# Optimization experiments

Hardware: AMD Instinct MI355X
Metric: run time of the kernel (lower is better)

## Reference

```python
import jax, jax.numpy as jnp
import numpy as np

OBS, ACT, H, B = 128, 32, 64, 32768
TMAX = 8  # max variable-length GRU steps: (15-1)//2+1 == 15//2+1 == 8
CENTER = 7


def gru_last(x_seq, valid, Wih, Whh, bih, bhh):
    """torch nn.GRU cell, masked scan; returns final hidden at each true length.
    x_seq: (B, TMAX, D), valid: (B, TMAX) bool. Gate order r, z, n."""
    Bn = x_seq.shape[0]
    h0 = jnp.zeros((Bn, Whh.shape[1]), x_seq.dtype)

    def step(h, inp):
        xt, vt = inp  # (B, D), (B,)
        gi = xt @ Wih.T + bih
        gh = h @ Whh.T + bhh
        ir, iz, inn = jnp.split(gi, 3, axis=-1)
        hr, hz, hn = jnp.split(gh, 3, axis=-1)
        r = jax.nn.sigmoid(ir + hr)
        zg = jax.nn.sigmoid(iz + hz)
        n = jnp.tanh(inn + r * hn)
        hnew = (1.0 - zg) * n + zg * h
        h = jnp.where(vt[:, None], hnew, h)
        return h, None

    h, _ = jax.lax.scan(step, h0, (jnp.swapaxes(x_seq, 0, 1), valid.T))
    return h


def setup_inputs() -> dict:
    key = jax.random.key(0)
    ks = jax.random.split(key, 20)
    def p(k, shape, s=0.05):
        return jax.random.normal(k, shape, jnp.float32) * s
    D = OBS + ACT
    return dict(
        obs_chunk=jax.random.normal(ks[0], (B, 15, OBS), jnp.float32),
        act_chunk=jax.random.normal(ks[1], (B, 15, ACT), jnp.float32),
        ln_g=jnp.ones((3,), jnp.float32), ln_b=jnp.zeros((3,), jnp.float32),
        dw1=p(ks[2], (16, 3)), db1=jnp.zeros((16,), jnp.float32),
        dw2=p(ks[3], (8, 16)), db2=jnp.zeros((8,), jnp.float32),
        dw3=p(ks[4], (14, 8)), db3=jnp.zeros((14,), jnp.float32),
        Wih_f=p(ks[5], (3 * H, D)), Whh_f=p(ks[6], (3 * H, H)),
        bih_f=jnp.zeros((3 * H,), jnp.float32), bhh_f=jnp.zeros((3 * H,), jnp.float32),
        Wih_b=p(ks[7], (3 * H, D)), Whh_b=p(ks[8], (3 * H, H)),
        bih_b=jnp.zeros((3 * H,), jnp.float32), bhh_b=jnp.zeros((3 * H,), jnp.float32),
        mw1=p(ks[9], (H, 2 * H)), mb1=jnp.zeros((H,), jnp.float32),
        mw2=p(ks[10], (H, H)), mb2=jnp.zeros((H,), jnp.float32),
        mu_w=p(ks[11], (H, H)), mu_b=jnp.zeros((H,), jnp.float32),
        lv_w=p(ks[12], (H, H)), lv_b=jnp.zeros((H,), jnp.float32),
    )


def reference(obs_chunk, act_chunk, ln_g, ln_b, dw1, db1, dw2, db2, dw3, db3,
              Wih_f, Whh_f, bih_f, bhh_f, Wih_b, Whh_b, bih_b, bhh_b,
              mw1, mb1, mw2, mb2, mu_w, mu_b, lv_w, lv_b):
    C = CENTER
    # --- DynamicTimeWindow features ---
    obs_t = obs_chunk[:, C]  # (B, OBS)
    pr = jax.nn.softmax(obs_t, axis=-1)
    entropy = -jnp.sum(pr * jnp.log(pr + 1e-8), axis=-1, keepdims=True)
    diffs = jnp.stack([jnp.linalg.norm(obs_chunk[:, C - k] - obs_chunk[:, C - k - 1], axis=-1)
                       for k in range(3)], axis=1)
    roc = diffs.mean(axis=1, keepdims=True)
    act_prev = act_chunk[:, C - 1]
    md = max(obs_t.shape[-1], act_prev.shape[-1])
    op = jnp.pad(obs_t, ((0, 0), (0, md - obs_t.shape[-1])))
    ap = jnp.pad(act_prev, ((0, 0), (0, md - act_prev.shape[-1])))
    oc = op - op.mean(axis=1, keepdims=True)
    ac = ap - ap.mean(axis=1, keepdims=True)
    denom = (jnp.linalg.norm(oc, axis=1, keepdims=True)
             * jnp.linalg.norm(ac, axis=1, keepdims=True) + 1e-8)
    corr = jnp.sum(oc * ac, axis=1, keepdims=True) / denom
    f = jnp.concatenate([entropy, roc, corr], axis=1)  # (B, 3)
    mean = f.mean(axis=-1, keepdims=True)
    var = f.var(axis=-1, keepdims=True)  # biased, matches torch LayerNorm
    fn = (f - mean) / jnp.sqrt(var + 1e-5) * ln_g + ln_b
    h1 = jax.nn.relu(fn @ dw1.T + db1)
    h2 = jax.nn.relu(h1 @ dw2.T + db2)
    logits = h2 @ dw3.T + db3  # (B, 14)
    widx = jnp.argmax(logits, axis=1)  # test_mode: argmax of softmax == argmax of logits
    wl = widx + 2  # window_len in [2, 15]
    idxs = jnp.arange(15)[None, :]
    start = (C - (wl - 1) // 2)[:, None]
    end = (C + wl // 2 + 1)[:, None]
    mask = ((idxs >= start) & (idxs < end)).astype(obs_chunk.dtype)  # (B, 15)
    x = jnp.concatenate([obs_chunk, act_chunk], axis=-1) * mask[..., None]  # (B, 15, D)
    # --- BiGRU over variable-length windows ---
    len_f = (wl - 1) // 2 + 1  # (B,)
    len_b = wl // 2 + 1
    t = jnp.arange(TMAX)
    idx_f = C - len_f[:, None] + 1 + t[None, :]  # left-aligned forward window
    idx_b = C + len_b[:, None] - 1 - t[None, :]  # reversed backward window
    seq_f = jnp.take_along_axis(x, idx_f[..., None], axis=1)  # (B, 8, D)
    seq_b = jnp.take_along_axis(x, idx_b[..., None], axis=1)
    vf = t[None, :] < len_f[:, None]
    vb = t[None, :] < len_b[:, None]
    h_f = gru_last(seq_f, vf, Wih_f, Whh_f, bih_f, bhh_f)  # (B, H)
    h_b = gru_last(seq_b, vb, Wih_b, Whh_b, bih_b, bhh_b)
    comb = jnp.concatenate([h_f, h_b], axis=1)  # (B, 2H)
    zenc = jax.nn.relu(comb @ mw1.T + mb1) @ mw2.T + mb2
    mu = zenc @ mu_w.T + mu_b
    sigma = jnp.exp(0.5 * (zenc @ lv_w.T + lv_b))
    z = mu  # test_mode=True
    return (z, mu, sigma)
```

## Files before the change

kernel.cpp:

```cpp
#include <hip/hip_runtime.h>

#define OBS 128
#define ACTD 32
#define DIMX 160
#define HID 64
#define NBATCH 32768
#define TMAXX 8
#define CTR 7
#define NPOS 15

typedef short bf16x8 __attribute__((ext_vector_type(8)));
typedef float f32x4 __attribute__((ext_vector_type(4)));

#define MFMA(a,b,c) __builtin_amdgcn_mfma_f32_16x16x32_bf16((a),(b),(c),0,0,0)

#define CTRL_BYTE 262144
#define SIDX_BYTE 278528
#define SIDX_CAP  66048
#define WB_BYTE   542720
#define COMB_BYTE 755712
#define NCB 64
#define EPB 512
#define HEAD_W_OFF 10752
#define TOTAL_SLOTS 13312

__device__ __forceinline__ unsigned short f2bf(float f) {
  unsigned u = __float_as_uint(f);
  return (unsigned short)((u + 0x7FFFu + ((u >> 16) & 1u)) >> 16);
}
__device__ __forceinline__ unsigned cvtpk(float a, float b) {
  unsigned r;
  asm("v_cvt_pk_bf16_f32 %0, %1, %2" : "=v"(r) : "v"(a), "v"(b));
  return r;
}

__device__ __forceinline__ float wsum(float v) {
#pragma unroll
  for (int s = 1; s < 64; s <<= 1) v += __shfl_xor(v, s);
  return v;
}
__device__ __forceinline__ float wmax(float v) {
#pragma unroll
  for (int s = 1; s < 64; s <<= 1) v = fmaxf(v, __shfl_xor(v, s));
  return v;
}

__global__ __launch_bounds__(256) void k_prep(
    const float* __restrict__ Wih_f, const float* __restrict__ Whh_f,
    const float* __restrict__ Wih_b, const float* __restrict__ Whh_b,
    const float* __restrict__ mw1, const float* __restrict__ mw2,
    const float* __restrict__ mu_w, const float* __restrict__ lv_w,
    unsigned short* __restrict__ dst) {
  int slot = blockIdx.x * 256 + threadIdx.x;
  if (slot >= TOTAL_SLOTS) return;
  const float* src;
  if (slot < HEAD_W_OFF) {
    int d = slot / 5376, r = slot % 5376;
    int f = r >> 8, rw = r & 255;
    int w = rw >> 6, lane = rw & 63;
    int col = lane & 15, kgrp = lane >> 4;
    int row = 16 * w + col;
    if (f < 15) {
      int g = f / 5, kf = f % 5;
      const float* W = d ? Wih_b : Wih_f;
      src = W + (size_t)(g * 64 + row) * 160 + kf * 32 + kgrp * 8;
    } else {
      int f2 = f - 15, g = f2 >> 1, kh = f2 & 1;
      const float* W = d ? Whh_b : Whh_f;
      src = W + (size_t)(g * 64 + row) * 64 + kh * 32 + kgrp * 8;
    }
  } else {
    int s2 = slot - HEAD_W_OFF;
    int f = s2 >> 8, rw = s2 & 255;
    int w = rw >> 6, lane = rw & 63;
    int col = lane & 15, kgrp = lane >> 4;
    int gr = 16 * w + col;
    if (f < 4)      src = mw1 + (size_t)gr * 128 + f * 32 + kgrp * 8;
    else if (f < 6) src = mw2 + (size_t)gr * 64 + (f - 4) * 32 + kgrp * 8;
    else if (f < 8) src = mu_w + (size_t)gr * 64 + (f - 6) * 32 + kgrp * 8;
    else            src = lv_w + (size_t)gr * 64 + (f - 8) * 32 + kgrp * 8;
  }
  unsigned short* o = dst + (size_t)slot * 8;
#pragma unroll
  for (int i = 0; i < 8; i++) o[i] = f2bf(src[i]);
}

__global__ __launch_bounds__(256) void k_decide(
    const float* __restrict__ obs, const float* __restrict__ act,
    const float* __restrict__ ln_g, const float* __restrict__ ln_b,
    const float* __restrict__ dw1, const float* __restrict__ db1,
    const float* __restrict__ dw2, const float* __restrict__ db2,
    const float* __restrict__ dw3, const float* __restrict__ db3,
    int* __restrict__ lens) {
  int b = blockIdx.x * 4 + (threadIdx.x >> 6);
  int l = threadIdx.x & 63;
  const float* o7 = obs + ((size_t)b * NPOS + CTR) * OBS;
  const float* o6 = o7 - OBS;
  const float* o5 = o7 - 2 * OBS;
  const float* o4 = o7 - 3 * OBS;
  float x0 = o7[l], x1 = o7[l + 64];
  float y60 = o6[l], y61 = o6[l + 64];
  float y50 = o5[l], y51 = o5[l + 64];
  float y40 = o4[l], y41 = o4[l + 64];
  float ap = (l < 32) ? act[((size_t)b * NPOS + 6) * ACTD + l] : 0.0f;

  float m = wmax(fmaxf(x0, x1));
  float e0 = expf(x0 - m), e1 = expf(x1 - m);
  float s = wsum(e0 + e1);
  float inv = 1.0f / s;
  float p0 = e0 * inv, p1 = e1 * inv;
  float ent = -wsum(p0 * logf(p0 + 1e-8f) + p1 * logf(p1 + 1e-8f));

  float d0 = wsum((x0 - y60) * (x0 - y60) + (x1 - y61) * (x1 - y61));
  float d1 = wsum((y60 - y50) * (y60 - y50) + (y61 - y51) * (y61 - y51));
  float d2 = wsum((y50 - y40) * (y50 - y40) + (y51 - y41) * (y51 - y41));
  float roc = (sqrtf(d0) + sqrtf(d1) + sqrtf(d2)) / 3.0f;

  float sop = wsum(x0 + x1);
  float sop2 = wsum(x0 * x0 + x1 * x1);
  float sap = wsum(ap);
  float sap2 = wsum(ap * ap);
  float dotoa = wsum(ap * x0);
  float mo = sop / 128.0f, ma = sap / 128.0f;
  float num = dotoa - 128.0f * mo * ma;
  float oc2 = fmaxf(sop2 - 128.0f * mo * mo, 0.0f);
  float ac2 = fmaxf(sap2 - 128.0f * ma * ma, 0.0f);
  float corr = num / (sqrtf(oc2) * sqrtf(ac2) + 1e-8f);

  float f0 = ent, f1 = roc, f2 = corr;
  float mean = (f0 + f1 + f2) / 3.0f;
  float v0 = f0 - mean, v1 = f1 - mean, v2 = f2 - mean;
  float var = (v0 * v0 + v1 * v1 + v2 * v2) / 3.0f;
  float sd = sqrtf(var + 1e-5f);
  float fn0 = v0 / sd * ln_g[0] + ln_b[0];
  float fn1 = v1 / sd * ln_g[1] + ln_b[1];
  float fn2 = v2 / sd * ln_g[2] + ln_b[2];

  float h1[16];
#pragma unroll
  for (int i = 0; i < 16; i++) {
    float a = db1[i] + fn0 * dw1[i * 3] + fn1 * dw1[i * 3 + 1] + fn2 * dw1[i * 3 + 2];
    h1[i] = fmaxf(a, 0.0f);
  }
  float h2[8];
#pragma unroll
  for (int i = 0; i < 8; i++) {
    float a = db2[i];
#pragma unroll
    for (int j = 0; j < 16; j++) a += h1[j] * dw2[i * 16 + j];
    h2[i] = fmaxf(a, 0.0f);
  }
  float best = -3.0e38f;
  int bi = 0;
#pragma unroll
  for (int i = 0; i < 14; i++) {
    float a = db3[i];
#pragma unroll
    for (int j = 0; j < 8; j++) a += h2[j] * dw3[i * 8 + j];
    if (a > best) { best = a; bi = i; }
  }
  int wl = bi + 2;
  if (l == 0) {
    lens[b] = (wl - 1) / 2 + 1;
    lens[NBATCH + b] = wl / 2 + 1;
  }
}

__global__ __launch_bounds__(256) void k_count(
    const int* __restrict__ lens, int* __restrict__ ctrl) {
  __shared__ int hist[16];
  const int tid = threadIdx.x, blk = blockIdx.x;
  if (tid < 16) hist[tid] = 0;
  __syncthreads();
#pragma unroll
  for (int j = 0; j < 2; j++) {
    int e = blk * EPB + j * 256 + tid;
    atomicAdd(&hist[lens[e] - 1], 1);
    atomicAdd(&hist[8 + lens[NBATCH + e] - 1], 1);
  }
  __syncthreads();
  if (tid < 16) ctrl[32 + 1024 + blk * 16 + tid] = hist[tid];
}

__global__ void k_scan(int* __restrict__ ctrl) {
  __shared__ int tot[16];
  __shared__ int pss[17];
  const int tid = threadIdx.x;
  const int* bh = ctrl + 32 + 1024;
  int* bb = ctrl + 32;
  if (tid < 16) {
    int s = 0;
    for (int blk = 0; blk < NCB; blk++) {
      bb[blk * 16 + tid] = s;
      s += bh[blk * 16 + tid];
    }
    tot[tid] = s;
  }
  __syncthreads();
  if (tid == 0) {
    int acc = 0;
    for (int k = 0; k < 16; k++) {
      pss[k] = acc;
      acc += (tot[k] + 31) & ~31;
    }
    pss[16] = acc;
    for (int k = 0; k < 17; k++) ctrl[k] = pss[k];
  }
  __syncthreads();
  if (tid < 16) {
    for (int blk = 0; blk < NCB; blk++) bb[blk * 16 + tid] += pss[tid];
  }
}

__global__ __launch_bounds__(256) void k_place(
    const int* __restrict__ lens, const int* __restrict__ ctrl,
    int* __restrict__ sidx) {
  __shared__ int hist[16];
  __shared__ int base[16];
  const int tid = threadIdx.x, blk = blockIdx.x;
  if (tid < 16) {
    hist[tid] = 0;
    base[tid] = ctrl[32 + blk * 16 + tid];
  }
  __syncthreads();
#pragma unroll
  for (int j = 0; j < 2; j++) {
    int e = blk * EPB + j * 256 + tid;
    int binf = lens[e] - 1;
    sidx[base[binf] + atomicAdd(&hist[binf], 1)] = e;
    int binb = 8 + lens[NBATCH + e] - 1;
    sidx[base[binb] + atomicAdd(&hist[binb], 1)] = e;
  }
}

__global__ __launch_bounds__(256, 2) void k_gru(
    const float* __restrict__ obs, const float* __restrict__ act,
    const int* __restrict__ ctrl, const int* __restrict__ sidx,
    const unsigned short* __restrict__ wbf,
    const float* __restrict__ bih_f, const float* __restrict__ bhh_f,
    const float* __restrict__ bih_b, const float* __restrict__ bhh_b,
    unsigned short* __restrict__ comb) {
  __shared__ unsigned short Xl[2][32 * 168];
  __shared__ unsigned short Hl[2][32 * 72];
  __shared__ int ei[32];

  const int tid = threadIdx.x;
  const int p = blockIdx.x * 32;
  const int* ps = ctrl;
  if (p >= ps[16]) return;
  int bin = 0;
#pragma unroll
  for (int k = 1; k < 16; k++) bin += (p >= ps[k]) ? 1 : 0;
  const int d = bin >> 3;
  const int len = (bin & 7) + 1;

  if (tid < 32) ei[tid] = sidx[p + tid];
  __syncthreads();

  const int w = tid >> 6, l = tid & 63;
  const int col = l & 15, kgrp = l >> 4;
  const int gr = 16 * w + col;

  const float* bih = d ? bih_b : bih_f;
  const float* bhh = d ? bhh_b : bhh_f;
  const float bias_r = bih[gr] + bhh[gr];
  const float bias_z = bih[64 + gr] + bhh[64 + gr];
  const float bias_in = bih[128 + gr];
  const float bias_hn = bhh[128 + gr];

  const unsigned short* fb = wbf + ((size_t)d * 5376 + tid) * 8;
  bf16x8 wr[5], wz[5], wn[5];
#pragma unroll
  for (int kf = 0; kf < 5; kf++) {
    wr[kf] = *(const bf16x8*)(fb + (size_t)kf * 2048);
    wz[kf] = *(const bf16x8*)(fb + (size_t)(5 + kf) * 2048);
    wn[kf] = *(const bf16x8*)(fb + (size_t)(10 + kf) * 2048);
  }
  bf16x8 vr[2], vz[2], vn[2];
#pragma unroll
  for (int kh = 0; kh < 2; kh++) {
    vr[kh] = *(const bf16x8*)(fb + (size_t)(15 + kh) * 2048);
    vz[kh] = *(const bf16x8*)(fb + (size_t)(17 + kh) * 2048);
    vn[kh] = *(const bf16x8*)(fb + (size_t)(19 + kh) * 2048);
  }

  const int p0 = d ? (CTR + len - 1) : (CTR - len + 1);
  const float* pst[5];
  int sstr[5], sdo[5];
#pragma unroll
  for (int it = 0; it < 5; it++) {
    int i = tid + it * 256;
    int eloc = i / 40;
    int q = i - eloc * 40;
    int eg = ei[eloc];
    if (eg < 0) eg = ei[0];
    if (q < 32) {
      pst[it] = obs + ((size_t)eg * NPOS + p0) * OBS + q * 4;
      sstr[it] = d ? -OBS : OBS;
    } else {
      pst[it] = act + ((size_t)eg * NPOS + p0) * ACTD + (q - 32) * 4;
      sstr[it] = d ? -ACTD : ACTD;
    }
    sdo[it] = eloc * 168 + ((q < 32) ? q * 4 : 128 + (q - 32) * 4);
  }
  float4 sv[5];

  auto stage_issue = [&](int t1) {
#pragma unroll
    for (int it = 0; it < 5; it++)
      sv[it] = *(const float4*)(pst[it] + (ptrdiff_t)t1 * sstr[it]);
  };
  auto stage_commit = [&](int buf) {
#pragma unroll
    for (int it = 0; it < 5; it++) {
      uint2 pk;
      pk.x = cvtpk(sv[it].x, sv[it].y);
      pk.y = cvtpk(sv[it].z, sv[it].w);
      *(uint2*)(&Xl[buf][sdo[it]]) = pk;
    }
  };

  stage_issue(0);
  stage_commit(0);
  __syncthreads();

  f32x4 hreg[2];
#pragma unroll
  for (int m = 0; m < 2; m++) hreg[m] = (f32x4){0.f, 0.f, 0.f, 0.f};

  for (int t = 0; t < len; t++) {
    const int cur = t & 1, nxt = cur ^ 1;
    const bool more = (t + 1 < len);
    if (more) stage_issue(t + 1);

    f32x4 ar[2], az[2], ain[2], ahn[2];
#pragma unroll
    for (int m = 0; m < 2; m++) {
      ar[m] = (f32x4){0.f, 0.f, 0.f, 0.f};
      az[m] = (f32x4){0.f, 0.f, 0.f, 0.f};
      ain[m] = (f32x4){0.f, 0.f, 0.f, 0.f};
      ahn[m] = (f32x4){0.f, 0.f, 0.f, 0.f};
    }
#pragma unroll
    for (int kf = 0; kf < 5; kf++) {
#pragma unroll
      for (int m = 0; m < 2; m++) {
        bf16x8 xa = *(const bf16x8*)(&Xl[cur][(col + 16 * m) * 168 + kf * 32 + kgrp * 8]);
        ar[m] = MFMA(xa, wr[kf], ar[m]);
        az[m] = MFMA(xa, wz[kf], az[m]);
        ain[m] = MFMA(xa, wn[kf], ain[m]);
      }
    }
    if (t > 0) {
#pragma unroll
      for (int kh = 0; kh < 2; kh++) {
#pragma unroll
        for (int m = 0; m < 2; m++) {
          bf16x8 ha = *(const bf16x8*)(&Hl[cur][(col + 16 * m) * 72 + kh * 32 + kgrp * 8]);
          ar[m] = MFMA(ha, vr[kh], ar[m]);
          az[m] = MFMA(ha, vz[kh], az[m]);
          ahn[m] = MFMA(ha, vn[kh], ahn[m]);
        }
      }
    }

#pragma unroll
    for (int m = 0; m < 2; m++) {
      float hvv[4];
#pragma unroll
      for (int r = 0; r < 4; r++) {
        float air = ar[m][r] + bias_r;
        float aiz = az[m][r] + bias_z;
        float rg = __builtin_amdgcn_rcpf(1.0f + __expf(-air));
        float zg = __builtin_amdgcn_rcpf(1.0f + __expf(-aiz));
        float nn = fmaf(rg, ahn[m][r] + bias_hn, ain[m][r] + bias_in);
        float th = fmaf(-2.0f, __builtin_amdgcn_rcpf(__expf(2.0f * nn) + 1.0f), 1.0f);
        float hp = hreg[m][r];
        float hv = fmaf(zg, hp - th, th);
        hreg[m][r] = hv;
        hvv[r] = hv;
      }
      if (more) {
        unsigned ua = cvtpk(hvv[0], hvv[1]);
        unsigned ub = cvtpk(hvv[2], hvv[3]);
        int row0 = (16 * m + kgrp * 4) * 72 + gr;
        Hl[nxt][row0] = (unsigned short)ua;
        Hl[nxt][row0 + 72] = (unsigned short)(ua >> 16);
        Hl[nxt][row0 + 144] = (unsigned short)ub;
        Hl[nxt][row0 + 216] = (unsigned short)(ub >> 16);
      }
    }

    if (more) {
      stage_commit(nxt);
      __syncthreads();
    }
  }

#pragma unroll
  for (int m = 0; m < 2; m++) {
#pragma unroll
    for (int r = 0; r < 4; r++) {
      int eg = ei[16 * m + kgrp * 4 + r];
      if (eg >= 0)
        comb[(size_t)eg * 128 + 64 * d + gr] = f2bf(hreg[m][r]);
    }
  }
}

__global__ __launch_bounds__(256) void k_head(
    const unsigned short* __restrict__ comb, const unsigned short* __restrict__ wbf,
    const float* __restrict__ mb1, const float* __restrict__ mb2,
    const float* __restrict__ mu_b, const float* __restrict__ lv_b,
    float* __restrict__ out) {
  __shared__ unsigned short Cl[64 * 136];
  __shared__ unsigned short Hl[64 * 72];
  __shared__ unsigned short Zl[64 * 72];

  const int tid = threadIdx.x;
  const int w = tid >> 6, l = tid & 63;
  const int col = l & 15, kgrp = l >> 4;
  const int gr = 16 * w + col;
  const int base = blockIdx.x * 64;

  {
    int row = tid >> 2, sq = tid & 3;
    const uint4* src = (const uint4*)(comb + (size_t)(base + row) * 128 + sq * 32);
    uint4* dst = (uint4*)(&Cl[row * 136 + sq * 32]);
#pragma unroll
    for (int j = 0; j < 4; j++) dst[j] = src[j];
  }
  __syncthreads();

  const unsigned short* hfb = wbf + ((size_t)HEAD_W_OFF + tid) * 8;
  const float b1 = mb1[gr], b2v = mb2[gr], bmu = mu_b[gr], blv = lv_b[gr];

  f32x4 t1[4];
#pragma unroll
  for (int m = 0; m < 4; m++) t1[m] = (f32x4){0.f, 0.f, 0.f, 0.f};
#pragma unroll
  for (int kf = 0; kf < 4; kf++) {
    bf16x8 bw = *(const bf16x8*)(hfb + (size_t)kf * 2048);
#pragma unroll
    for (int m = 0; m < 4; m++) {
      bf16x8 ca = *(const bf16x8*)(&Cl[(col + 16 * m) * 136 + kf * 32 + kgrp * 8]);
      t1[m] = MFMA(ca, bw, t1[m]);
    }
  }
#pragma unroll
  for (int m = 0; m < 4; m++) {
#pragma unroll
    for (int r = 0; r < 4; r++) {
      float v = fmaxf(t1[m][r] + b1, 0.0f);
      Hl[(16 * m + kgrp * 4 + r) * 72 + gr] = f2bf(v);
    }
  }
  __syncthreads();

  f32x4 ze[4];
#pragma unroll
  for (int m = 0; m < 4; m++) ze[m] = (f32x4){0.f, 0.f, 0.f, 0.f};
#pragma unroll
  for (int kh = 0; kh < 2; kh++) {
    bf16x8 bw = *(const bf16x8*)(hfb + (size_t)(4 + kh) * 2048);
#pragma unroll
    for (int m = 0; m < 4; m++) {
      bf16x8 ha = *(const bf16x8*)(&Hl[(col + 16 * m) * 72 + kh * 32 + kgrp * 8]);
      ze[m] = MFMA(ha, bw, ze[m]);
    }
  }
#pragma unroll
  for (int m = 0; m < 4; m++) {
#pragma unroll
    for (int r = 0; r < 4; r++) {
      Zl[(16 * m + kgrp * 4 + r) * 72 + gr] = f2bf(ze[m][r] + b2v);
    }
  }
  __syncthreads();

  f32x4 amu[4], alv[4];
#pragma unroll
  for (int m = 0; m < 4; m++) {
    amu[m] = (f32x4){0.f, 0.f, 0.f, 0.f};
    alv[m] = (f32x4){0.f, 0.f, 0.f, 0.f};
  }
#pragma unroll
  for (int kh = 0; kh < 2; kh++) {
    bf16x8 bwm = *(const bf16x8*)(hfb + (size_t)(6 + kh) * 2048);
    bf16x8 bwl = *(const bf16x8*)(hfb + (size_t)(8 + kh) * 2048);
#pragma unroll
    for (int m = 0; m < 4; m++) {
      bf16x8 za = *(const bf16x8*)(&Zl[(col + 16 * m) * 72 + kh * 32 + kgrp * 8]);
      amu[m] = MFMA(za, bwm, amu[m]);
      alv[m] = MFMA(za, bwl, alv[m]);
    }
  }
#pragma unroll
  for (int m = 0; m < 4; m++) {
#pragma unroll
    for (int r = 0; r < 4; r++) {
      int e = 16 * m + kgrp * 4 + r;
      float mu = amu[m][r] + bmu;
      float sg = expf(0.5f * (alv[m][r] + blv));
      size_t o = (size_t)(base + e) * HID + gr;
      out[o] = mu;
      out[(size_t)NBATCH * HID + o] = mu;
      out[2 * (size_t)NBATCH * HID + o] = sg;
    }
  }
}

extern "C" void kernel_launch(void* const* d_in, const int* in_sizes, int n_in,
                              void* d_out, int out_size, void* d_ws, size_t ws_size,
                              hipStream_t stream) {
  const float* obs = (const float*)d_in[0];
  const float* act = (const float*)d_in[1];
  const float* ln_g = (const float*)d_in[2];
  const float* ln_b = (const float*)d_in[3];
  const float* dw1 = (const float*)d_in[4];
  const float* db1 = (const float*)d_in[5];
  const float* dw2 = (const float*)d_in[6];
  const float* db2 = (const float*)d_in[7];
  const float* dw3 = (const float*)d_in[8];
  const float* db3 = (const float*)d_in[9];
  const float* Wih_f = (const float*)d_in[10];
  const float* Whh_f = (const float*)d_in[11];
  const float* bih_f = (const float*)d_in[12];
  const float* bhh_f = (const float*)d_in[13];
  const float* Wih_b = (const float*)d_in[14];
  const float* Whh_b = (const float*)d_in[15];
  const float* bih_b = (const float*)d_in[16];
  const float* bhh_b = (const float*)d_in[17];
  const float* mw1 = (const float*)d_in[18];
  const float* mb1 = (const float*)d_in[19];
  const float* mw2 = (const float*)d_in[20];
  const float* mb2 = (const float*)d_in[21];
  const float* mu_w = (const float*)d_in[22];
  const float* mu_b = (const float*)d_in[23];
  const float* lv_w = (const float*)d_in[24];
  const float* lv_b = (const float*)d_in[25];

  int* lens = (int*)d_ws;
  int* ctrl = (int*)((char*)d_ws + CTRL_BYTE);
  int* sidx = (int*)((char*)d_ws + SIDX_BYTE);
  unsigned short* wbf = (unsigned short*)((char*)d_ws + WB_BYTE);
  unsigned short* comb = (unsigned short*)((char*)d_ws + COMB_BYTE);

  hipMemsetAsync(sidx, 0xFF, SIDX_CAP * sizeof(int), stream);

  k_prep<<<(TOTAL_SLOTS + 255) / 256, 256, 0, stream>>>(
      Wih_f, Whh_f, Wih_b, Whh_b, mw1, mw2, mu_w, lv_w, wbf);
  k_decide<<<NBATCH / 4, 256, 0, stream>>>(obs, act, ln_g, ln_b, dw1, db1, dw2,
                                           db2, dw3, db3, lens);
  k_count<<<NCB, 256, 0, stream>>>(lens, ctrl);
  k_scan<<<1, 64, 0, stream>>>(ctrl);
  k_place<<<NCB, 256, 0, stream>>>(lens, ctrl, sidx);
  k_gru<<<SIDX_CAP / 32, 256, 0, stream>>>(obs, act, ctrl, sidx, wbf, bih_f,
                                           bhh_f, bih_b, bhh_b, comb);
  k_head<<<NBATCH / 64, 256, 0, stream>>>(comb, wbf, mb1, mb2, mu_b, lv_b,
                                          (float*)d_out);
}
```

Measured before the change: 127.0 us.

## Widen GRU tiles to 64 sequences, fill padding in scan, simplify entropy

The GRU kernel now handles 64 sequences per block instead of 32, so each wave runs four MFMA row tiles per preloaded weight fragment. Bins are padded to multiples of 64 to match, and the sidx padding slots are filled with -1 inside k_scan, which replaces the full-buffer memset. The entropy in k_decide is rewritten as log(s) - sum(e*(x-m))/s using fast intrinsics, removing per-element logs. The tradeoffs are doubled LDS and staging registers, which can lower occupancy, more wasted padding rows, and fewer blocks in flight.

```diff
diff --git a/kernel.cpp b/kernel.cpp
--- a/kernel.cpp
+++ b/kernel.cpp
@@ -16,9 +16,9 @@
 
 #define CTRL_BYTE 262144
 #define SIDX_BYTE 278528
-#define SIDX_CAP  66048
-#define WB_BYTE   542720
-#define COMB_BYTE 755712
+#define SIDX_CAP  66560
+#define WB_BYTE   544768
+#define COMB_BYTE 757760
 #define NCB 64
 #define EPB 512
 #define HEAD_W_OFF 10752
@@ -105,11 +105,10 @@
   float ap = (l < 32) ? act[((size_t)b * NPOS + 6) * ACTD + l] : 0.0f;
 
   float m = wmax(fmaxf(x0, x1));
-  float e0 = expf(x0 - m), e1 = expf(x1 - m);
+  float e0 = __expf(x0 - m), e1 = __expf(x1 - m);
   float s = wsum(e0 + e1);
-  float inv = 1.0f / s;
-  float p0 = e0 * inv, p1 = e1 * inv;
-  float ent = -wsum(p0 * logf(p0 + 1e-8f) + p1 * logf(p1 + 1e-8f));
+  float dot = wsum(e0 * (x0 - m) + e1 * (x1 - m));
+  float ent = __logf(s) - dot / s;
 
   float d0 = wsum((x0 - y60) * (x0 - y60) + (x1 - y61) * (x1 - y61));
   float d1 = wsum((y60 - y50) * (y60 - y50) + (y61 - y51) * (y61 - y51));
@@ -182,7 +181,7 @@
   if (tid < 16) ctrl[32 + 1024 + blk * 16 + tid] = hist[tid];
 }
 
-__global__ void k_scan(int* __restrict__ ctrl) {
+__global__ void k_scan(int* __restrict__ ctrl, int* __restrict__ sidx) {
   __shared__ int tot[16];
   __shared__ int pss[17];
   const int tid = threadIdx.x;
@@ -201,7 +200,7 @@
     int acc = 0;
     for (int k = 0; k < 16; k++) {
       pss[k] = acc;
-      acc += (tot[k] + 31) & ~31;
+      acc += (tot[k] + 63) & ~63;
     }
     pss[16] = acc;
     for (int k = 0; k < 17; k++) ctrl[k] = pss[k];
@@ -209,6 +208,11 @@
   __syncthreads();
   if (tid < 16) {
     for (int blk = 0; blk < NCB; blk++) bb[blk * 16 + tid] += pss[tid];
+  }
+  __syncthreads();
+  for (int k = 0; k < 16; k++) {
+    int s = pss[k] + tot[k], e2 = pss[k + 1];
+    for (int i = s + tid; i < e2; i += 64) sidx[i] = -1;
   }
 }
 
@@ -240,12 +244,12 @@
     const float* __restrict__ bih_f, const float* __restrict__ bhh_f,
     const float* __restrict__ bih_b, const float* __restrict__ bhh_b,
     unsigned short* __restrict__ comb) {
-  __shared__ unsigned short Xl[2][32 * 168];
-  __shared__ unsigned short Hl[2][32 * 72];
-  __shared__ int ei[32];
+  __shared__ unsigned short Xl[2][64 * 168];
+  __shared__ unsigned short Hl[2][64 * 72];
+  __shared__ int ei[64];
 
   const int tid = threadIdx.x;
-  const int p = blockIdx.x * 32;
+  const int p = blockIdx.x * 64;
   const int* ps = ctrl;
   if (p >= ps[16]) return;
   int bin = 0;
@@ -254,7 +258,7 @@
   const int d = bin >> 3;
   const int len = (bin & 7) + 1;
 
-  if (tid < 32) ei[tid] = sidx[p + tid];
+  if (tid < 64) ei[tid] = sidx[p + tid];
   __syncthreads();
 
   const int w = tid >> 6, l = tid & 63;
@@ -285,34 +289,42 @@
   }
 
   const int p0 = d ? (CTR + len - 1) : (CTR - len + 1);
-  const float* pst[5];
-  int sstr[5], sdo[5];
-#pragma unroll
-  for (int it = 0; it < 5; it++) {
+  int soff[10];
+  int sdo[10];
+  unsigned qmask = 0;
+#pragma unroll
+  for (int it = 0; it < 10; it++) {
     int i = tid + it * 256;
     int eloc = i / 40;
     int q = i - eloc * 40;
     int eg = ei[eloc];
     if (eg < 0) eg = ei[0];
     if (q < 32) {
-      pst[it] = obs + ((size_t)eg * NPOS + p0) * OBS + q * 4;
-      sstr[it] = d ? -OBS : OBS;
+      soff[it] = eg * (NPOS * OBS) + p0 * OBS + q * 4;
+      qmask |= 1u << it;
+      sdo[it] = eloc * 168 + q * 4;
     } else {
-      pst[it] = act + ((size_t)eg * NPOS + p0) * ACTD + (q - 32) * 4;
-      sstr[it] = d ? -ACTD : ACTD;
-    }
-    sdo[it] = eloc * 168 + ((q < 32) ? q * 4 : 128 + (q - 32) * 4);
-  }
-  float4 sv[5];
+      soff[it] = eg * (NPOS * ACTD) + p0 * ACTD + (q - 32) * 4;
+      sdo[it] = eloc * 168 + 128 + (q - 32) * 4;
+    }
+  }
+  const int sA = d ? -OBS : OBS;
+  const int sB = d ? -ACTD : ACTD;
+  float4 sv[10];
 
   auto stage_issue = [&](int t1) {
-#pragma unroll
-    for (int it = 0; it < 5; it++)
-      sv[it] = *(const float4*)(pst[it] + (ptrdiff_t)t1 * sstr[it]);
+    int offA = t1 * sA, offB = t1 * sB;
+#pragma unroll
+    for (int it = 0; it < 10; it++) {
+      bool isObs = (qmask >> it) & 1u;
+      const float* bp = isObs ? obs : act;
+      int o = soff[it] + (isObs ? offA : offB);
+      sv[it] = *(const float4*)(bp + o);
+    }
   };
   auto stage_commit = [&](int buf) {
 #pragma unroll
-    for (int it = 0; it < 5; it++) {
+    for (int it = 0; it < 10; it++) {
       uint2 pk;
       pk.x = cvtpk(sv[it].x, sv[it].y);
       pk.y = cvtpk(sv[it].z, sv[it].w);
@@ -324,56 +336,45 @@
   stage_commit(0);
   __syncthreads();
 
-  f32x4 hreg[2];
-#pragma unroll
-  for (int m = 0; m < 2; m++) hreg[m] = (f32x4){0.f, 0.f, 0.f, 0.f};
+  f32x4 hreg[4];
+#pragma unroll
+  for (int m = 0; m < 4; m++) hreg[m] = (f32x4){0.f, 0.f, 0.f, 0.f};
 
   for (int t = 0; t < len; t++) {
     const int cur = t & 1, nxt = cur ^ 1;
     const bool more = (t + 1 < len);
     if (more) stage_issue(t + 1);
 
-    f32x4 ar[2], az[2], ain[2], ahn[2];
-#pragma unroll
-    for (int m = 0; m < 2; m++) {
-      ar[m] = (f32x4){0.f, 0.f, 0.f, 0.f};
-      az[m] = (f32x4){0.f, 0.f, 0.f, 0.f};
-      ain[m] = (f32x4){0.f, 0.f, 0.f, 0.f};
-      ahn[m] = (f32x4){0.f, 0.f, 0.f, 0.f};
-    }
-#pragma unroll
-    for (int kf = 0; kf < 5; kf++) {
-#pragma unroll
-      for (int m = 0; m < 2; m++) {
+#pragma unroll
+    for (int m = 0; m < 4; m++) {
+      f32x4 ar = (f32x4){0.f, 0.f, 0.f, 0.f};
+      f32x4 az = (f32x4){0.f, 0.f, 0.f, 0.f};
+      f32x4 ain = (f32x4){0.f, 0.f, 0.f, 0.f};
+      f32x4 ahn = (f32x4){0.f, 0.f, 0.f, 0.f};
+#pragma unroll
+      for (int kf = 0; kf < 5; kf++) {
         bf16x8 xa = *(const bf16x8*)(&Xl[cur][(col + 16 * m) * 168 + kf * 32 + kgrp * 8]);
-        ar[m] = MFMA(xa, wr[kf], ar[m]);
-        az[m] = MFMA(xa, wz[kf], az[m]);
-        ain[m] = MFMA(xa, wn[kf], ain[m]);
+        ar = MFMA(xa, wr[kf], ar);
+        az = MFMA(xa, wz[kf], az);
+        ain = MFMA(xa, wn[kf], ain);
       }
-    }
-    if (t > 0) {
-#pragma unroll
-      for (int kh = 0; kh < 2; kh++) {
-#pragma unroll
-        for (int m = 0; m < 2; m++) {
+      if (t > 0) {
+#pragma unroll
+        for (int kh = 0; kh < 2; kh++) {
           bf16x8 ha = *(const bf16x8*)(&Hl[cur][(col + 16 * m) * 72 + kh * 32 + kgrp * 8]);
-          ar[m] = MFMA(ha, vr[kh], ar[m]);
-          az[m] = MFMA(ha, vz[kh], az[m]);
-          ahn[m] = MFMA(ha, vn[kh], ahn[m]);
+          ar = MFMA(ha, vr[kh], ar);
+          az = MFMA(ha, vz[kh], az);
+          ahn = MFMA(ha, vn[kh], ahn);
         }
       }
-    }
-
-#pragma unroll
-    for (int m = 0; m < 2; m++) {
       float hvv[4];
 #pragma unroll
       for (int r = 0; r < 4; r++) {
-        float air = ar[m][r] + bias_r;
-        float aiz = az[m][r] + bias_z;
+        float air = ar[r] + bias_r;
+        float aiz = az[r] + bias_z;
         float rg = __builtin_amdgcn_rcpf(1.0f + __expf(-air));
         float zg = __builtin_amdgcn_rcpf(1.0f + __expf(-aiz));
-        float nn = fmaf(rg, ahn[m][r] + bias_hn, ain[m][r] + bias_in);
+        float nn = fmaf(rg, ahn[r] + bias_hn, ain[r] + bias_in);
         float th = fmaf(-2.0f, __builtin_amdgcn_rcpf(__expf(2.0f * nn) + 1.0f), 1.0f);
         float hp = hreg[m][r];
         float hv = fmaf(zg, hp - th, th);
@@ -398,7 +399,7 @@
   }
 
 #pragma unroll
-  for (int m = 0; m < 2; m++) {
+  for (int m = 0; m < 4; m++) {
 #pragma unroll
     for (int r = 0; r < 4; r++) {
       int eg = ei[16 * m + kgrp * 4 + r];
@@ -546,16 +547,14 @@
   unsigned short* wbf = (unsigned short*)((char*)d_ws + WB_BYTE);
   unsigned short* comb = (unsigned short*)((char*)d_ws + COMB_BYTE);
 
-  hipMemsetAsync(sidx, 0xFF, SIDX_CAP * sizeof(int), stream);
-
   k_prep<<<(TOTAL_SLOTS + 255) / 256, 256, 0, stream>>>(
       Wih_f, Whh_f, Wih_b, Whh_b, mw1, mw2, mu_w, lv_w, wbf);
   k_decide<<<NBATCH / 4, 256, 0, stream>>>(obs, act, ln_g, ln_b, dw1, db1, dw2,
                                            db2, dw3, db3, lens);
   k_count<<<NCB, 256, 0, stream>>>(lens, ctrl);
-  k_scan<<<1, 64, 0, stream>>>(ctrl);
+  k_scan<<<1, 64, 0, stream>>>(ctrl, sidx);
   k_place<<<NCB, 256, 0, stream>>>(lens, ctrl, sidx);
-  k_gru<<<SIDX_CAP / 32, 256, 0, stream>>>(obs, act, ctrl, sidx, wbf, bih_f,
+  k_gru<<<SIDX_CAP / 64, 256, 0, stream>>>(obs, act, ctrl, sidx, wbf, bih_f,
                                            bhh_f, bih_b, bhh_b, comb);
   k_head<<<NBATCH / 64, 256, 0, stream>>>(comb, wbf, mb1, mb2, mu_b, lv_b,
                                           (float*)d_out);
```

After: 133.9 us. +5.4%, slower.
